# Kernel optimization log

Hardware: AMD Instinct MI355X
Metric: run time of the kernel (lower is better)

## Reference

```python
import jax, jax.numpy as jnp
import numpy as np

N_HEAD = 16
EPS = 1e-6


def setup_inputs() -> dict:
    key = jax.random.key(0)
    k1, k2, k3 = jax.random.split(key, 3)
    B, T, C = 2, 2048, 1024
    x = jax.random.normal(k1, (B, T, C), dtype=jnp.float32)
    w_attn = jax.random.normal(k2, (C, 3 * C), dtype=jnp.float32) * 0.02
    w_proj = jax.random.normal(k3, (C, C), dtype=jnp.float32) * 0.02
    return {"x": x, "w_attn": w_attn, "w_proj": w_proj}


def _linear_attention(q, k, v):
    """q,k,v: (T,B,H,D) with q,k already feature-mapped (elu+1).
    Causal linear attention via a D x D running-state recurrence (same math
    as cumsum of k-v outer products, computed without the O(T*D^2) tensor)."""
    B, H, D = q.shape[1], q.shape[2], q.shape[3]

    def step(carry, qkv_t):
        S, z = carry                      # S:(B,H,D,D), z:(B,H,D)
        qt, kt, vt = qkv_t                # each (B,H,D)
        S = S + kt[..., :, None] * vt[..., None, :]
        z = z + kt
        num = jnp.einsum('bhi,bhij->bhj', qt, S)
        den = jnp.sum(qt * z, axis=-1, keepdims=True)
        return (S, z), num / (den + EPS)

    S0 = jnp.zeros((B, H, D, D), q.dtype)
    z0 = jnp.zeros((B, H, D), q.dtype)
    _, y = jax.lax.scan(step, (S0, z0), (q, k, v))
    return y                              # (T,B,H,D)


def reference(x, w_attn, w_proj):
    B, T, C = x.shape
    H = N_HEAD
    D = C // H
    qkv = x @ w_attn                      # (B,T,3C)
    q, k, v = jnp.split(qkv, 3, axis=-1)

    def to_tbhd(a):                       # (B,T,C) -> (T,B,H,D)
        return a.reshape(B, T, H, D).transpose(1, 0, 2, 3)

    q = jax.nn.elu(to_tbhd(q)) + 1.0      # phi(x) = ELU(x)+1
    k = jax.nn.elu(to_tbhd(k)) + 1.0
    v = to_tbhd(v)

    y = _linear_attention(q, k, v)        # (T,B,H,D)
    y = y.transpose(1, 0, 2, 3).reshape(B, T, C)
    return y @ w_proj                     # resid dropout p=0.0 is identity
```

## Files before the change

### kernel.cpp

```cpp
#include <hip/hip_runtime.h>
#include <hip/hip_bf16.h>
#include <cmath>

#define TB   2048
#define CCH  1024
#define NCH  32
#define EPSF 1e-6f

typedef unsigned short u16;
typedef __attribute__((ext_vector_type(8))) short  frag8;
typedef __attribute__((ext_vector_type(4))) float  floatx4;

__device__ __forceinline__ u16 f2bf(float f) {
    unsigned int u = __float_as_uint(f);
    unsigned int r = (u + 0x7fffu + ((u >> 16) & 1u)) >> 16;
    return (u16)r;
}
__device__ __forceinline__ float bf2f(u16 v) {
    return __uint_as_float(((unsigned int)v) << 16);
}

__device__ __forceinline__ void async_load16(const u16* g, u16* l) {
    __builtin_amdgcn_global_load_lds(
        (const __attribute__((address_space(1))) void*)g,
        (__attribute__((address_space(3))) void*)l,
        16, 0, 0);
}

__global__ __launch_bounds__(256) void prep_k(
    const float* __restrict__ x, const float* __restrict__ wa,
    const float* __restrict__ wp,
    u16* __restrict__ xb, u16* __restrict__ waT, u16* __restrict__ wpT)
{
    __shared__ u16 t[64][72];
    int blk = blockIdx.x;
    if (blk < 2048) {
        int i = (blk * 256 + threadIdx.x) * 8;
        float4 a = *(const float4*)(x + i);
        float4 b = *(const float4*)(x + i + 4);
        u16 v[8];
        v[0] = f2bf(a.x); v[1] = f2bf(a.y); v[2] = f2bf(a.z); v[3] = f2bf(a.w);
        v[4] = f2bf(b.x); v[5] = f2bf(b.y); v[6] = f2bf(b.z); v[7] = f2bf(b.w);
        *(uint4*)(xb + i) = *(uint4*)v;
        return;
    }
    const float* in; u16* out; int K, N, bx, by;
    if (blk < 2048 + 768) {
        int tb = blk - 2048; in = wa; out = waT; K = 1024; N = 3072;
        bx = tb % 48; by = tb / 48;
    } else {
        int tb = blk - 2816; in = wp; out = wpT; K = 1024; N = 1024;
        bx = tb & 15; by = tb >> 4;
    }
    const int k0 = by * 64, n0 = bx * 64;
    #pragma unroll
    for (int i = 0; i < 4; ++i) {
        int rr = (threadIdx.x >> 4) + 16 * i;
        int c4 = (threadIdx.x & 15) * 4;
        float4 v = *(const float4*)(in + (size_t)(k0 + rr) * N + n0 + c4);
        t[c4 + 0][rr] = f2bf(v.x);
        t[c4 + 1][rr] = f2bf(v.y);
        t[c4 + 2][rr] = f2bf(v.z);
        t[c4 + 3][rr] = f2bf(v.w);
    }
    __syncthreads();
    #pragma unroll
    for (int i = 0; i < 2; ++i) {
        int rr = (threadIdx.x >> 3) + 32 * i;
        int c8 = (threadIdx.x & 7) * 8;
        u16 o[8];
        #pragma unroll
        for (int q = 0; q < 8; ++q) o[q] = t[rr][c8 + q];
        *(uint4*)(out + (size_t)(n0 + rr) * K + k0 + c8) = *(uint4*)o;
    }
}

__global__ __launch_bounds__(256) void gemm_bf16_bf16out_k(
    const u16* __restrict__ A, const u16* __restrict__ BT,
    u16* __restrict__ C, int N, int K, int phi_cols)
{
    __shared__ u16 Als[128 * 64];
    __shared__ u16 Bls[128 * 64];
    const int tid  = threadIdx.x;
    const int wave = tid >> 6, lane = tid & 63;
    const int quad = lane >> 4, lrow = lane & 15;
    const int wm = wave >> 1, wn = wave & 1;
    const int row0 = blockIdx.y * 128, col0 = blockIdx.x * 128;
    const int lr = lane >> 3;
    const int lc = ((lane & 7) ^ lr) * 8;
    const int rsw = lrow & 7;
    floatx4 acc[4][4] = {};

    for (int k0 = 0; k0 < K; k0 += 64) {
        __syncthreads();
        #pragma unroll
        for (int m = 0; m < 4; ++m) {
            int i = wave * 4 + m;
            async_load16(A  + (size_t)(row0 + i * 8 + lr) * K + k0 + lc, &Als[i * 512]);
            async_load16(BT + (size_t)(col0 + i * 8 + lr) * K + k0 + lc, &Bls[i * 512]);
        }
        __syncthreads();
        #pragma unroll
        for (int ksi = 0; ksi < 2; ++ksi) {
            frag8 af[4], bf[4];
            #pragma unroll
            for (int i = 0; i < 4; ++i)
                af[i] = *(const frag8*)&Als[(wm * 64 + i * 16 + lrow) * 64
                                            + ((ksi * 4 + quad) ^ rsw) * 8];
            #pragma unroll
            for (int i = 0; i < 4; ++i)
                bf[i] = *(const frag8*)&Bls[(wn * 64 + i * 16 + lrow) * 64
                                            + ((ksi * 4 + quad) ^ rsw) * 8];
            #pragma unroll
            for (int i = 0; i < 4; ++i)
                #pragma unroll
                for (int jn = 0; jn < 4; ++jn)
                    acc[i][jn] = __builtin_amdgcn_mfma_f32_16x16x32_bf16(
                        af[i], bf[jn], acc[i][jn], 0, 0, 0);
        }
    }

    #pragma unroll
    for (int i = 0; i < 4; ++i) {
        #pragma unroll
        for (int jn = 0; jn < 4; ++jn) {
            int col = col0 + wn * 64 + jn * 16 + lrow;
            bool isphi = col < phi_cols;
            #pragma unroll
            for (int r = 0; r < 4; ++r) {
                int row = row0 + wm * 64 + i * 16 + quad * 4 + r;
                float v = acc[i][jn][r];
                if (isphi) v = (v > 0.f) ? (v + 1.f) : __expf(v);
                C[(size_t)row * N + col] = f2bf(v);
            }
        }
    }
}

__global__ __launch_bounds__(256) void gemm_bf16_f32out_k(
    const u16* __restrict__ A, const u16* __restrict__ BT,
    float* __restrict__ C, int N, int K)
{
    __shared__ u16 Als[128 * 128];
    __shared__ u16 Bls[64 * 128];
    const int tid  = threadIdx.x;
    const int wave = tid >> 6, lane = tid & 63;
    const int quad = lane >> 4, lrow = lane & 15;
    const int wm = wave >> 1, wn = wave & 1;
    const int row0 = blockIdx.y * 128, col0 = blockIdx.x * 64;
    const int lr4 = lane >> 4;
    floatx4 acc[4][2] = {};

    for (int k0 = 0; k0 < K; k0 += 128) {
        __syncthreads();
        #pragma unroll
        for (int m = 0; m < 8; ++m) {
            int rbase = wave * 32 + m * 4;
            int cg = (lane & 15) ^ ((rbase + lr4) & 15);
            async_load16(A + (size_t)(row0 + rbase + lr4) * K + k0 + cg * 8,
                         &Als[rbase * 128]);
        }
        #pragma unroll
        for (int m = 0; m < 4; ++m) {
            int rbase = wave * 16 + m * 4;
            int cg = (lane & 15) ^ ((rbase + lr4) & 15);
            async_load16(BT + (size_t)(col0 + rbase + lr4) * K + k0 + cg * 8,
                         &Bls[rbase * 128]);
        }
        __syncthreads();
        #pragma unroll
        for (int ksi = 0; ksi < 4; ++ksi) {
            frag8 af[4], bf[2];
            #pragma unroll
            for (int i = 0; i < 4; ++i)
                af[i] = *(const frag8*)&Als[(wm * 64 + i * 16 + lrow) * 128
                                            + ((ksi * 4 + quad) ^ lrow) * 8];
            #pragma unroll
            for (int jn = 0; jn < 2; ++jn)
                bf[jn] = *(const frag8*)&Bls[(wn * 32 + jn * 16 + lrow) * 128
                                             + ((ksi * 4 + quad) ^ lrow) * 8];
            #pragma unroll
            for (int i = 0; i < 4; ++i)
                #pragma unroll
                for (int jn = 0; jn < 2; ++jn)
                    acc[i][jn] = __builtin_amdgcn_mfma_f32_16x16x32_bf16(
                        af[i], bf[jn], acc[i][jn], 0, 0, 0);
        }
    }

    #pragma unroll
    for (int i = 0; i < 4; ++i)
        #pragma unroll
        for (int jn = 0; jn < 2; ++jn) {
            int col = col0 + wn * 32 + jn * 16 + lrow;
            #pragma unroll
            for (int r = 0; r < 4; ++r) {
                int row = row0 + wm * 64 + i * 16 + quad * 4 + r;
                C[(size_t)row * N + col] = acc[i][jn][r];
            }
        }
}

__global__ __launch_bounds__(256) void chunk_kv_mfma_k(
    const u16* __restrict__ qkv,
    u16* __restrict__ Spt,
    float* __restrict__ zloc)
{
    __shared__ u16 Kt[64][72];
    __shared__ u16 Vt[64][72];
    const int tid  = threadIdx.x;
    const int wave = tid >> 6, lane = tid & 63;
    const int quad = lane >> 4, lrow = lane & 15;
    const int blk = blockIdx.x;
    const int c = blk & 31, h = (blk >> 5) & 15, b = blk >> 9;
    const int t0 = c * 64;
    const u16* base = qkv + (size_t)(b * TB + t0) * 3072 + h * 64;

    #pragma unroll
    for (int m = 0; m < 2; ++m) {
        int chunk = tid + 256 * m;
        int s = chunk >> 3, d0 = (chunk & 7) * 8;
        const u16* row = base + (size_t)s * 3072;
        u16 kv[8], vv[8];
        *(uint4*)kv = *(const uint4*)(row + 1024 + d0);
        *(uint4*)vv = *(const uint4*)(row + 2048 + d0);
        #pragma unroll
        for (int q = 0; q < 8; ++q) { Kt[d0 + q][s] = kv[q]; Vt[d0 + q][s] = vv[q]; }
    }
    __syncthreads();

    frag8 vf[2];
    #pragma unroll
    for (int ks = 0; ks < 2; ++ks)
        vf[ks] = *(const frag8*)&Vt[wave * 16 + lrow][ks * 32 + quad * 8];
    u16* So = Spt + (size_t)blk * 4096;
    #pragma unroll
    for (int jn = 0; jn < 4; ++jn) {
        floatx4 acc = {};
        #pragma unroll
        for (int ks = 0; ks < 2; ++ks) {
            frag8 kf = *(const frag8*)&Kt[jn * 16 + lrow][ks * 32 + quad * 8];
            acc = __builtin_amdgcn_mfma_f32_16x16x32_bf16(vf[ks], kf, acc, 0, 0, 0);
        }
        #pragma unroll
        for (int r = 0; r < 4; ++r) {
            int j = wave * 16 + quad * 4 + r;
            int i = jn * 16 + lrow;
            So[j * 64 + i] = f2bf(acc[r]);
        }
    }
    if (tid < 64) {
        float z = 0.f;
        for (int s = 0; s < 64; ++s) z += bf2f(Kt[tid][s]);
        zloc[(size_t)blk * 64 + tid] = z;
    }
}

__global__ __launch_bounds__(256) void scan_state_k(
    u16* __restrict__ Spt, float* __restrict__ z)
{
    const int bh = blockIdx.x >> 1;
    const int part = blockIdx.x & 1;
    const int e0 = part * 2048 + threadIdx.x * 8;
    const size_t base = (size_t)bh * NCH * 4096;
    float r[8] = {};
    for (int c = 0; c < NCH; ++c) {
        u16* p = Spt + base + (size_t)c * 4096 + e0;
        u16 t[8];
        *(uint4*)t = *(const uint4*)p;
        u16 o[8];
        #pragma unroll
        for (int q = 0; q < 8; ++q) { o[q] = f2bf(r[q]); r[q] += bf2f(t[q]); }
        *(uint4*)p = *(uint4*)o;
    }
    if (part == 0 && threadIdx.x < 64) {
        const size_t zb = (size_t)bh * NCH * 64;
        float rz = 0.f;
        for (int c = 0; c < NCH; ++c) {
            float t = z[zb + c * 64 + threadIdx.x];
            z[zb + c * 64 + threadIdx.x] = rz;
            rz += t;
        }
    }
}

__global__ __launch_bounds__(256) void attn_mfma_k(
    const u16* __restrict__ qkv,
    const u16* __restrict__ SptG,
    const float* __restrict__ zp,
    u16* __restrict__ Yb)
{
    __shared__ u16 Qs[64][72];
    __shared__ u16 Ks[64][72];
    __shared__ u16 Vt[64][72];
    __shared__ u16 Sp[64][72];
    __shared__ float zps[64];
    __shared__ float den4[64][4];
    __shared__ float den[64];

    const int tid  = threadIdx.x;
    const int wave = tid >> 6, lane = tid & 63;
    const int quad = lane >> 4, lrow = lane & 15;
    const int blk = blockIdx.x;
    const int c = blk & 31, h = (blk >> 5) & 15, b = blk >> 9;
    const int t0 = c * 64;
    const u16* base = qkv + (size_t)(b * TB + t0) * 3072 + h * 64;

    #pragma unroll
    for (int m = 0; m < 2; ++m) {
        int chunk = tid + 256 * m;
        int s = chunk >> 3, d0 = (chunk & 7) * 8;
        const u16* row = base + (size_t)s * 3072;
        *(uint4*)&Qs[s][d0] = *(const uint4*)(row + d0);
        *(uint4*)&Ks[s][d0] = *(const uint4*)(row + 1024 + d0);
        u16 vv[8];
        *(uint4*)vv = *(const uint4*)(row + 2048 + d0);
        #pragma unroll
        for (int q = 0; q < 8; ++q) Vt[d0 + q][s] = vv[q];
        *(uint4*)&Sp[s][d0] = *(const uint4*)(SptG + (size_t)blk * 4096 + chunk * 8);
    }
    if (tid < 64) zps[tid] = zp[(size_t)blk * 64 + tid];
    __syncthreads();

    frag8 qf[2];
    #pragma unroll
    for (int ks = 0; ks < 2; ++ks)
        qf[ks] = *(const frag8*)&Qs[wave * 16 + lrow][ks * 32 + quad * 8];

    floatx4 yacc[4] = {}, kacc[4] = {};
    #pragma unroll
    for (int jn = 0; jn < 4; ++jn) {
        #pragma unroll
        for (int ks = 0; ks < 2; ++ks) {
            frag8 spf = *(const frag8*)&Sp[jn * 16 + lrow][ks * 32 + quad * 8];
            yacc[jn] = __builtin_amdgcn_mfma_f32_16x16x32_bf16(qf[ks], spf, yacc[jn], 0, 0, 0);
            frag8 kf = *(const frag8*)&Ks[jn * 16 + lrow][ks * 32 + quad * 8];
            kacc[jn] = __builtin_amdgcn_mfma_f32_16x16x32_bf16(qf[ks], kf, kacc[jn], 0, 0, 0);
        }
    }
    __syncthreads();

    #pragma unroll
    for (int jn = 0; jn < 4; ++jn) {
        int s = jn * 16 + lrow;
        #pragma unroll
        for (int r = 0; r < 4; ++r) {
            int t = wave * 16 + quad * 4 + r;
            float v = (s <= t) ? kacc[jn][r] : 0.f;
            Sp[t][s] = f2bf(v);
        }
    }
    __syncthreads();

    {
        int t = tid >> 2, seg = tid & 3;
        float p = 0.f;
        #pragma unroll
        for (int i = 0; i < 16; ++i) {
            int d = seg * 16 + i;
            p += bf2f(Qs[t][d]) * zps[d] + bf2f(Sp[t][d]);
        }
        den4[t][seg] = p;
    }

    frag8 af2[2];
    #pragma unroll
    for (int ks = 0; ks < 2; ++ks)
        af2[ks] = *(const frag8*)&Sp[wave * 16 + lrow][ks * 32 + quad * 8];
    #pragma unroll
    for (int jn = 0; jn < 4; ++jn)
        #pragma unroll
        for (int ks = 0; ks < 2; ++ks) {
            frag8 vf = *(const frag8*)&Vt[jn * 16 + lrow][ks * 32 + quad * 8];
            yacc[jn] = __builtin_amdgcn_mfma_f32_16x16x32_bf16(af2[ks], vf, yacc[jn], 0, 0, 0);
        }
    __syncthreads();
    if (tid < 64) den[tid] = den4[tid][0] + den4[tid][1] + den4[tid][2] + den4[tid][3];
    __syncthreads();

    #pragma unroll
    for (int jn = 0; jn < 4; ++jn) {
        #pragma unroll
        for (int r = 0; r < 4; ++r) {
            int t = wave * 16 + quad * 4 + r;
            float inv = 1.f / (den[t] + EPSF);
            Qs[t][jn * 16 + lrow] = f2bf(yacc[jn][r] * inv);
        }
    }
    __syncthreads();
    {
        int row = tid >> 2, seg = tid & 3;
        size_t o = (size_t)(b * TB + t0 + row) * CCH + h * 64 + seg * 16;
        *(uint4*)(Yb + o)     = *(uint4*)&Qs[row][seg * 16];
        *(uint4*)(Yb + o + 8) = *(uint4*)&Qs[row][seg * 16 + 8];
    }
}

extern "C" void kernel_launch(void* const* d_in, const int* in_sizes, int n_in,
                              void* d_out, int out_size, void* d_ws, size_t ws_size,
                              hipStream_t stream)
{
    const float* x      = (const float*)d_in[0];
    const float* w_attn = (const float*)d_in[1];
    const float* w_proj = (const float*)d_in[2];
    float* out = (float*)d_out;

    u16* xb    = (u16*)d_ws;
    u16* waT   = xb    + (size_t)4096 * 1024;
    u16* wpT   = waT   + (size_t)3072 * 1024;
    u16* Yb    = wpT   + (size_t)1024 * 1024;
    u16* qkv_b = Yb    + (size_t)4096 * 1024;
    u16* Spt   = qkv_b + (size_t)4096 * 3072;
    float* zloc = (float*)(Spt + (size_t)1024 * 4096);

    prep_k<<<3072, 256, 0, stream>>>(x, w_attn, w_proj, xb, waT, wpT);

    gemm_bf16_bf16out_k<<<dim3(24, 32), 256, 0, stream>>>(xb, waT, qkv_b, 3072, 1024, 2048);

    chunk_kv_mfma_k<<<1024, 256, 0, stream>>>(qkv_b, Spt, zloc);
    scan_state_k   <<<64,   256, 0, stream>>>(Spt, zloc);
    attn_mfma_k    <<<1024, 256, 0, stream>>>(qkv_b, Spt, zloc, Yb);

    gemm_bf16_f32out_k<<<dim3(16, 32), 256, 0, stream>>>(Yb, wpT, out, 1024, 1024);
}
```

Baseline: 169.7 us.

## Fuse state scan into chunk kernel via ticket counters; async swizzled LDS loads

```diff
diff --git a/kernel.cpp b/kernel.cpp
--- a/kernel.cpp
+++ b/kernel.cpp
@@ -204,10 +204,13 @@
 __global__ __launch_bounds__(256) void chunk_kv_mfma_k(
     const u16* __restrict__ qkv,
     u16* __restrict__ Spt,
-    float* __restrict__ zloc)
+    float* __restrict__ zloc,
+    u16* __restrict__ VtG,
+    unsigned int* __restrict__ tickets)
 {
     __shared__ u16 Kt[64][72];
     __shared__ u16 Vt[64][72];
+    __shared__ unsigned int s_old;
     const int tid  = threadIdx.x;
     const int wave = tid >> 6, lane = tid & 63;
     const int quad = lane >> 4, lrow = lane & 15;
@@ -229,6 +232,16 @@
     }
     __syncthreads();
 
+    #pragma unroll
+    for (int m = 0; m < 2; ++m) {
+        int e = tid + 256 * m;
+        int r = e >> 3, c8 = (e & 7) * 8;
+        u16 o[8];
+        #pragma unroll
+        for (int q = 0; q < 8; ++q) o[q] = Vt[r][c8 + q];
+        *(uint4*)(VtG + (size_t)blk * 4096 + r * 64 + c8) = *(uint4*)o;
+    }
+
     frag8 vf[2];
     #pragma unroll
     for (int ks = 0; ks < 2; ++ks)
@@ -254,32 +267,38 @@
         for (int s = 0; s < 64; ++s) z += bf2f(Kt[tid][s]);
         zloc[(size_t)blk * 64 + tid] = z;
     }
-}
-
-__global__ __launch_bounds__(256) void scan_state_k(
-    u16* __restrict__ Spt, float* __restrict__ z)
-{
-    const int bh = blockIdx.x >> 1;
-    const int part = blockIdx.x & 1;
-    const int e0 = part * 2048 + threadIdx.x * 8;
-    const size_t base = (size_t)bh * NCH * 4096;
-    float r[8] = {};
-    for (int c = 0; c < NCH; ++c) {
-        u16* p = Spt + base + (size_t)c * 4096 + e0;
-        u16 t[8];
-        *(uint4*)t = *(const uint4*)p;
-        u16 o[8];
-        #pragma unroll
-        for (int q = 0; q < 8; ++q) { o[q] = f2bf(r[q]); r[q] += bf2f(t[q]); }
-        *(uint4*)p = *(uint4*)o;
-    }
-    if (part == 0 && threadIdx.x < 64) {
-        const size_t zb = (size_t)bh * NCH * 64;
-        float rz = 0.f;
-        for (int c = 0; c < NCH; ++c) {
-            float t = z[zb + c * 64 + threadIdx.x];
-            z[zb + c * 64 + threadIdx.x] = rz;
-            rz += t;
+
+    __threadfence();
+    __syncthreads();
+    if (tid == 0) s_old = atomicAdd(&tickets[blk >> 5], 1u);
+    __syncthreads();
+    if (s_old == 31u) {
+        __threadfence();
+        const int bh = blk >> 5;
+        const size_t sbase = (size_t)bh * NCH * 4096;
+        float r0[8] = {}, r1[8] = {};
+        for (int cc = 0; cc < NCH; ++cc) {
+            u16* p0 = Spt + sbase + (size_t)cc * 4096 + tid * 8;
+            u16* p1 = p0 + 2048;
+            u16 t0v[8], t1v[8], o0[8], o1[8];
+            *(uint4*)t0v = *(const uint4*)p0;
+            *(uint4*)t1v = *(const uint4*)p1;
+            #pragma unroll
+            for (int q = 0; q < 8; ++q) {
+                o0[q] = f2bf(r0[q]); r0[q] += bf2f(t0v[q]);
+                o1[q] = f2bf(r1[q]); r1[q] += bf2f(t1v[q]);
+            }
+            *(uint4*)p0 = *(uint4*)o0;
+            *(uint4*)p1 = *(uint4*)o1;
+        }
+        if (tid < 64) {
+            const size_t zb = (size_t)bh * NCH * 64;
+            float rz = 0.f;
+            for (int cc = 0; cc < NCH; ++cc) {
+                float tv = zloc[zb + cc * 64 + tid];
+                zloc[zb + cc * 64 + tid] = rz;
+                rz += tv;
+            }
         }
     }
 }
@@ -288,12 +307,13 @@
     const u16* __restrict__ qkv,
     const u16* __restrict__ SptG,
     const float* __restrict__ zp,
+    const u16* __restrict__ VtG,
     u16* __restrict__ Yb)
 {
-    __shared__ u16 Qs[64][72];
-    __shared__ u16 Ks[64][72];
-    __shared__ u16 Vt[64][72];
-    __shared__ u16 Sp[64][72];
+    __shared__ u16 Qls[64 * 64];
+    __shared__ u16 Kls[64 * 64];
+    __shared__ u16 Vls[64 * 64];
+    __shared__ u16 Sls[64 * 64];
     __shared__ float zps[64];
     __shared__ float den4[64][4];
     __shared__ float den[64];
@@ -304,20 +324,19 @@
     const int blk = blockIdx.x;
     const int c = blk & 31, h = (blk >> 5) & 15, b = blk >> 9;
     const int t0 = c * 64;
-    const u16* base = qkv + (size_t)(b * TB + t0) * 3072 + h * 64;
+    const int lr = lane >> 3;
+    const int lc = ((lane & 7) ^ lr) * 8;
+    const int rsw = lrow & 7;
+    const u16* qbase = qkv + (size_t)(b * TB + t0) * 3072 + h * 64;
 
     #pragma unroll
     for (int m = 0; m < 2; ++m) {
-        int chunk = tid + 256 * m;
-        int s = chunk >> 3, d0 = (chunk & 7) * 8;
-        const u16* row = base + (size_t)s * 3072;
-        *(uint4*)&Qs[s][d0] = *(const uint4*)(row + d0);
-        *(uint4*)&Ks[s][d0] = *(const uint4*)(row + 1024 + d0);
-        u16 vv[8];
-        *(uint4*)vv = *(const uint4*)(row + 2048 + d0);
-        #pragma unroll
-        for (int q = 0; q < 8; ++q) Vt[d0 + q][s] = vv[q];
-        *(uint4*)&Sp[s][d0] = *(const uint4*)(SptG + (size_t)blk * 4096 + chunk * 8);
+        int i = wave * 2 + m;
+        int r = i * 8 + lr;
+        async_load16(qbase + (size_t)r * 3072 + lc,          &Qls[i * 512]);
+        async_load16(qbase + (size_t)r * 3072 + 1024 + lc,   &Kls[i * 512]);
+        async_load16(SptG + (size_t)blk * 4096 + r * 64 + lc, &Sls[i * 512]);
+        async_load16(VtG  + (size_t)blk * 4096 + r * 64 + lc, &Vls[i * 512]);
     }
     if (tid < 64) zps[tid] = zp[(size_t)blk * 64 + tid];
     __syncthreads();
@@ -325,16 +344,16 @@
     frag8 qf[2];
     #pragma unroll
     for (int ks = 0; ks < 2; ++ks)
-        qf[ks] = *(const frag8*)&Qs[wave * 16 + lrow][ks * 32 + quad * 8];
+        qf[ks] = *(const frag8*)&Qls[(wave * 16 + lrow) * 64 + ((ks * 4 + quad) ^ rsw) * 8];
 
     floatx4 yacc[4] = {}, kacc[4] = {};
     #pragma unroll
     for (int jn = 0; jn < 4; ++jn) {
         #pragma unroll
         for (int ks = 0; ks < 2; ++ks) {
-            frag8 spf = *(const frag8*)&Sp[jn * 16 + lrow][ks * 32 + quad * 8];
+            frag8 spf = *(const frag8*)&Sls[(jn * 16 + lrow) * 64 + ((ks * 4 + quad) ^ rsw) * 8];
             yacc[jn] = __builtin_amdgcn_mfma_f32_16x16x32_bf16(qf[ks], spf, yacc[jn], 0, 0, 0);
-            frag8 kf = *(const frag8*)&Ks[jn * 16 + lrow][ks * 32 + quad * 8];
+            frag8 kf = *(const frag8*)&Kls[(jn * 16 + lrow) * 64 + ((ks * 4 + quad) ^ rsw) * 8];
             kacc[jn] = __builtin_amdgcn_mfma_f32_16x16x32_bf16(qf[ks], kf, kacc[jn], 0, 0, 0);
         }
     }
@@ -347,7 +366,7 @@
         for (int r = 0; r < 4; ++r) {
             int t = wave * 16 + quad * 4 + r;
             float v = (s <= t) ? kacc[jn][r] : 0.f;
-            Sp[t][s] = f2bf(v);
+            Sls[t * 64 + (((s >> 3) ^ (t & 7)) * 8) + (s & 7)] = f2bf(v);
         }
     }
     __syncthreads();
@@ -356,9 +375,15 @@
         int t = tid >> 2, seg = tid & 3;
         float p = 0.f;
         #pragma unroll
-        for (int i = 0; i < 16; ++i) {
-            int d = seg * 16 + i;
-            p += bf2f(Qs[t][d]) * zps[d] + bf2f(Sp[t][d]);
+        for (int g2 = 0; g2 < 2; ++g2) {
+            int g = seg * 2 + g2;
+            int pq = ((g ^ (t & 7)) * 8);
+            const u16* qp = &Qls[t * 64 + pq];
+            const u16* ap = &Sls[t * 64 + pq];
+            #pragma unroll
+            for (int e = 0; e < 8; ++e) {
+                p += bf2f(qp[e]) * zps[g * 8 + e] + bf2f(ap[e]);
+            }
         }
         den4[t][seg] = p;
     }
@@ -366,12 +391,12 @@
     frag8 af2[2];
     #pragma unroll
     for (int ks = 0; ks < 2; ++ks)
-        af2[ks] = *(const frag8*)&Sp[wave * 16 + lrow][ks * 32 + quad * 8];
+        af2[ks] = *(const frag8*)&Sls[(wave * 16 + lrow) * 64 + ((ks * 4 + quad) ^ rsw) * 8];
     #pragma unroll
     for (int jn = 0; jn < 4; ++jn)
         #pragma unroll
         for (int ks = 0; ks < 2; ++ks) {
-            frag8 vf = *(const frag8*)&Vt[jn * 16 + lrow][ks * 32 + quad * 8];
+            frag8 vf = *(const frag8*)&Vls[(jn * 16 + lrow) * 64 + ((ks * 4 + quad) ^ rsw) * 8];
             yacc[jn] = __builtin_amdgcn_mfma_f32_16x16x32_bf16(af2[ks], vf, yacc[jn], 0, 0, 0);
         }
     __syncthreads();
@@ -384,15 +409,15 @@
         for (int r = 0; r < 4; ++r) {
             int t = wave * 16 + quad * 4 + r;
             float inv = 1.f / (den[t] + EPSF);
-            Qs[t][jn * 16 + lrow] = f2bf(yacc[jn][r] * inv);
+            Qls[t * 64 + jn * 16 + lrow] = f2bf(yacc[jn][r] * inv);
         }
     }
     __syncthreads();
     {
         int row = tid >> 2, seg = tid & 3;
         size_t o = (size_t)(b * TB + t0 + row) * CCH + h * 64 + seg * 16;
-        *(uint4*)(Yb + o)     = *(uint4*)&Qs[row][seg * 16];
-        *(uint4*)(Yb + o + 8) = *(uint4*)&Qs[row][seg * 16 + 8];
+        *(uint4*)(Yb + o)     = *(uint4*)&Qls[row * 64 + seg * 16];
+        *(uint4*)(Yb + o + 8) = *(uint4*)&Qls[row * 64 + seg * 16 + 8];
     }
 }
 
@@ -411,15 +436,19 @@
     u16* Yb    = wpT   + (size_t)1024 * 1024;
     u16* qkv_b = Yb    + (size_t)4096 * 1024;
     u16* Spt   = qkv_b + (size_t)4096 * 3072;
-    float* zloc = (float*)(Spt + (size_t)1024 * 4096);
+    u16* VtG   = Spt   + (size_t)1024 * 4096;
+    float* zloc = (float*)(VtG + (size_t)1024 * 4096);
+    unsigned int* tickets = (unsigned int*)(zloc + (size_t)1024 * 64);
+
+    hipMemsetAsync(tickets, 0, 32 * sizeof(unsigned int), stream);
 
     prep_k<<<3072, 256, 0, stream>>>(x, w_attn, w_proj, xb, waT, wpT);
 
     gemm_bf16_bf16out_k<<<dim3(24, 32), 256, 0, stream>>>(xb, waT, qkv_b, 3072, 1024, 2048);
 
-    chunk_kv_mfma_k<<<1024, 256, 0, stream>>>(qkv_b, Spt, zloc);
-    scan_state_k   <<<64,   256, 0, stream>>>(Spt, zloc);
-    attn_mfma_k    <<<1024, 256, 0, stream>>>(qkv_b, Spt, zloc, Yb);
+    chunk_kv_mfma_k<<<1024, 256, 0, stream>>>(qkv_b, Spt, zloc, VtG, tickets);
+
+    attn_mfma_k<<<1024, 256, 0, stream>>>(qkv_b, Spt, zloc, VtG, Yb);
 
     gemm_bf16_f32out_k<<<dim3(16, 32), 256, 0, stream>>>(Yb, wpT, out, 1024, 1024);
 }
```

Result: slower. 319.8 us (+88.5%).
